# Performance work log

Hardware: AMD Instinct MI355X
Metric: run time of the kernel (lower is better)

## Reference

```python
import jax, jax.numpy as jnp
import numpy as np

NUM_HEADS = 16
LN_EPS = 1e-5


def pos_encoding(length, d):
    pos = jnp.arange(length, dtype=jnp.float32)[:, None]
    i = jnp.arange(d, dtype=jnp.float32)[None, :]
    angle = pos / jnp.power(10000.0, (2.0 * jnp.floor(i / 2.0)) / d)
    return jnp.where((jnp.arange(d) % 2) == 0, jnp.sin(angle), jnp.cos(angle))


def rel_shift(x):
    # x: (B, H, l, m) -> TXL shift trick
    b, h, l, m = x.shape
    x = jnp.concatenate([x, jnp.zeros((b, h, l, 1), x.dtype)], axis=-1)
    x = x.reshape(b, h, l * (m + 1))
    return x[:, :, l - 1:-1].reshape(b, h, l, m)


def layer_norm(x, g, b):
    mu = jnp.mean(x, axis=-1, keepdims=True)
    var = jnp.mean(jnp.square(x - mu), axis=-1, keepdims=True)
    return (x - mu) * jax.lax.rsqrt(var + LN_EPS) * g + b


def setup_inputs() -> dict:
    key = jax.random.key(0)
    B, S, M, D, L, V = 2, 1024, 1024, 1024, 4, 32000
    ks = jax.random.split(key, 32)
    s = 0.02
    d = {
        'inputs': jax.random.randint(ks[0], (B, S), 0, V, dtype=jnp.int32),
        'mems': jax.random.normal(ks[1], (L, B, M, D), jnp.float32),
        'emb': jax.random.normal(ks[2], (V, D), jnp.float32) * s,
        'Wq': jax.random.normal(ks[3], (L, D, D), jnp.float32) * s,
        'bq': jnp.zeros((L, D), jnp.float32),
        'Wke': jax.random.normal(ks[4], (L, D, D), jnp.float32) * s,
        'bke': jnp.zeros((L, D), jnp.float32),
        'Wkr': jax.random.normal(ks[5], (L, D, D), jnp.float32) * s,
        'bkr': jnp.zeros((L, D), jnp.float32),
        'Wv': jax.random.normal(ks[6], (L, D, D), jnp.float32) * s,
        'bv': jnp.zeros((L, D), jnp.float32),
        'Wo': jax.random.normal(ks[7], (L, D, D), jnp.float32) * s,
        'bo': jnp.zeros((L, D), jnp.float32),
        'ln1_g': jnp.ones((L, D), jnp.float32),
        'ln1_b': jnp.zeros((L, D), jnp.float32),
        'W1': jax.random.normal(ks[8], (L, D, D), jnp.float32) * s,
        'b1': jnp.zeros((L, D), jnp.float32),
        'W2': jax.random.normal(ks[9], (L, D, D), jnp.float32) * s,
        'b2': jnp.zeros((L, D), jnp.float32),
        'ln2_g': jnp.ones((L, D), jnp.float32),
        'ln2_b': jnp.zeros((L, D), jnp.float32),
        'Wh': jax.random.normal(ks[10], (D, D), jnp.float32) * s,
        'bh': jnp.zeros((D,), jnp.float32),
        'Wf': jax.random.normal(ks[11], (D, V), jnp.float32) * s,
        'bf': jnp.zeros((V,), jnp.float32),
        'next_mem_len': 1024,
    }
    return d


def reference(inputs, mems, emb, Wq, bq, Wke, bke, Wkr, bkr, Wv, bv, Wo, bo,
              ln1_g, ln1_b, W1, b1, W2, b2, ln2_g, ln2_b, Wh, bh, Wf, bf,
              next_mem_len):
    B, S = inputs.shape
    L, _, M, D = mems.shape
    T = M + S
    H = NUM_HEADS
    dh = D // H
    sqrt_dk = jnp.sqrt(jnp.float32(dh))

    rel_enc = pos_encoding(T, D)[::-1]  # (T, D), reversed
    # look-ahead mask: query i may attend key j iff j <= i + M
    mask = (jnp.arange(T)[None, :] > (jnp.arange(S)[:, None] + M)).astype(jnp.float32)
    mask = mask[None, None] * -1e9  # (1,1,S,T)

    x = emb[inputs] * jnp.sqrt(jnp.float32(D))  # (B,S,D)

    for l in range(L):
        x_tilde = jnp.concatenate([mems[l], x], axis=1)  # (B,T,D)
        q = (x @ Wq[l] + bq[l]).reshape(B, S, H, dh).transpose(0, 2, 1, 3)
        k = (x_tilde @ Wke[l] + bke[l]).reshape(B, T, H, dh).transpose(0, 2, 1, 3)
        v = (x_tilde @ Wv[l] + bv[l]).reshape(B, T, H, dh).transpose(0, 2, 1, 3)
        A = jnp.einsum('bhsd,bhtd->bhst', q, k)
        Qr = (rel_enc @ Wkr[l] + bkr[l]).reshape(T, H, dh).transpose(1, 0, 2)  # (H,T,dh)
        B_hat = jnp.einsum('bhsd,htd->bhst', q, Qr)
        score = (A + rel_shift(B_hat)) / sqrt_dk + mask
        attn = jax.nn.softmax(score, axis=-1)
        ctx = jnp.einsum('bhst,bhtd->bhsd', attn, v)
        ctx = ctx.transpose(0, 2, 1, 3).reshape(B, S, D)
        attn_out = ctx @ Wo[l] + bo[l]
        h1 = layer_norm(x + attn_out, ln1_g[l], ln1_b[l])
        ff = jax.nn.gelu(h1 @ W1[l] + b1[l], approximate=False) @ W2[l] + b2[l]
        x = layer_norm(h1 + ff, ln2_g[l], ln2_b[l])

    x = jax.nn.gelu(x @ Wh + bh, approximate=False)
    logits = x @ Wf + bf
    return logits
```

## Files before the change

### kernel.cpp

```cpp
#include <hip/hip_runtime.h>
#include <hip/hip_bf16.h>
#include <math.h>

typedef __attribute__((ext_vector_type(4))) float f32x4;
typedef __attribute__((ext_vector_type(8))) short s16x8;

#define BB 2
#define SS 1024
#define MEM 1024
#define DD 1024
#define LL 4
#define VV 32000
#define TT 2048
#define NH 16
#define DH 64

__device__ __forceinline__ short f2bf(float f) {
    unsigned u = __float_as_uint(f);
    u += 0x7fffu + ((u >> 16) & 1u);
    return (short)(u >> 16);
}

__device__ __forceinline__ float gelu_f(float x) {
    return 0.5f * x * (1.0f + erff(x * 0.70710678118654752f));
}

__device__ __forceinline__ void gll16(const short* g, short* l) {
    __builtin_amdgcn_global_load_lds(
        (__attribute__((address_space(1))) void*)(short*)g,
        (__attribute__((address_space(3))) void*)l, 16, 0, 0);
}

template<int WM, int WN>
__global__ __launch_bounds__(256) void gemm_k128(
    const short* __restrict__ A, const short* __restrict__ Bt,
    const float* __restrict__ bias, const float* __restrict__ bias2,
    int nsplit, void* __restrict__ Cv, int N, int K, int nby, int act, int obf)
{
    constexpr int BM = WM * 32, BN = WN * 32;
    constexpr int NA = BM / 16, NB = BN / 16;
    __shared__ short a_s[BM * 128];
    __shared__ short b_s[BN * 128];
    const int tid  = threadIdx.x;
    const int lane = tid & 63;
    const int wave = tid >> 6;
    const int wr = wave >> 1, wc = wave & 1;
    const int fr = lane & 15, fg = lane >> 4;

    const int nwg = gridDim.x;
    const int bid = blockIdx.x;
    const int swz = ((nwg & 7) == 0) ? ((bid & 7) * (nwg >> 3) + (bid >> 3)) : bid;
    const size_t m0 = (size_t)(swz % nby) * BM;
    const size_t n0 = (size_t)(swz / nby) * BN;

    const short* gA[NA]; short* lA[NA];
    const short* gB[NB]; short* lB[NB];
    #pragma unroll
    for (int i = 0; i < NA; ++i) {
        gA[i] = A + (m0 + i * 16 + (tid & 15)) * (size_t)K + (tid >> 4) * 8;
        lA[i] = &a_s[(i * 256 + tid) * 8];
    }
    #pragma unroll
    for (int i = 0; i < NB; ++i) {
        gB[i] = Bt + (n0 + i * 16 + (tid & 15)) * (size_t)K + (tid >> 4) * 8;
        lB[i] = &b_s[(i * 256 + tid) * 8];
    }

    f32x4 acc[WM][WN] = {};

    #pragma unroll
    for (int i = 0; i < NA; ++i) gll16(gA[i], lA[i]);
    #pragma unroll
    for (int i = 0; i < NB; ++i) gll16(gB[i], lB[i]);

    const int nt = K >> 7;
    for (int t = 0; t < nt; ++t) {
        __syncthreads();
        s16x8 af[WM][4], bf[WN][4];
        #pragma unroll
        for (int mi = 0; mi < WM; ++mi)
            #pragma unroll
            for (int h = 0; h < 4; ++h)
                af[mi][h] = *(const s16x8*)&a_s[((wr*WM + mi)*256 + (4*h + fg)*16 + fr) * 8];
        #pragma unroll
        for (int ni = 0; ni < WN; ++ni)
            #pragma unroll
            for (int h = 0; h < 4; ++h)
                bf[ni][h] = *(const s16x8*)&b_s[((wc*WN + ni)*256 + (4*h + fg)*16 + fr) * 8];
        if (t + 1 < nt) {
            __syncthreads();
            const int koff = (t + 1) << 7;
            #pragma unroll
            for (int i = 0; i < NA; ++i) gll16(gA[i] + koff, lA[i]);
            #pragma unroll
            for (int i = 0; i < NB; ++i) gll16(gB[i] + koff, lB[i]);
        }
        #pragma unroll
        for (int mi = 0; mi < WM; ++mi)
            #pragma unroll
            for (int ni = 0; ni < WN; ++ni)
                #pragma unroll
                for (int h = 0; h < 4; ++h)
                    acc[mi][ni] = __builtin_amdgcn_mfma_f32_16x16x32_bf16(
                        af[mi][h], bf[ni][h], acc[mi][ni], 0, 0, 0);
    }

    float* Cf = (float*)Cv;
    short* Cb = (short*)Cv;
    #pragma unroll
    for (int mi = 0; mi < WM; ++mi) {
        #pragma unroll
        for (int ni = 0; ni < WN; ++ni) {
            const size_t r0 = m0 + wr*WM*16 + mi*16 + fg*4;
            const size_t c  = n0 + wc*WN*16 + ni*16 + fr;
            const float bb = (c < (size_t)nsplit) ? bias[c] : bias2[c - nsplit];
            #pragma unroll
            for (int rg = 0; rg < 4; ++rg) {
                float vv = acc[mi][ni][rg] + bb;
                if (act) vv = gelu_f(vv);
                if (obf) Cb[(r0 + rg)*(size_t)N + c] = f2bf(vv);
                else     Cf[(r0 + rg)*(size_t)N + c] = vv;
            }
        }
    }
}

#define READ_A8(MH, BUF) \
  _Pragma("unroll") for (int mf = 0; mf < 4; ++mf) \
  _Pragma("unroll") for (int kh = 0; kh < 2; ++kh) \
    aA[mf][kh] = *(const s16x8*)&lds[(BUF)*16384 + WR*8192 + (((MH)*4+mf)*128 + (kh*4+fg)*16 + fr)*8];

#define READ_B8(BUF) \
  _Pragma("unroll") for (int nf = 0; nf < 4; ++nf) \
  _Pragma("unroll") for (int kh = 0; kh < 2; ++kh) \
    bB[nf][kh] = *(const s16x8*)&lds[32768 + (BUF)*16384 + BH*8192 + ((BC4+nf)*128 + (kh*4+fg)*16 + fr)*8];

#define QUAD8(MH, NHX) \
  _Pragma("unroll") for (int mf = 0; mf < 4; ++mf) \
  _Pragma("unroll") for (int n2 = 0; n2 < 2; ++n2) { \
    acc[(MH)*4+mf][(NHX)*2+n2] = __builtin_amdgcn_mfma_f32_16x16x32_bf16( \
        aA[mf][0], bB[(NHX)*2+n2][0], acc[(MH)*4+mf][(NHX)*2+n2], 0, 0, 0); \
    acc[(MH)*4+mf][(NHX)*2+n2] = __builtin_amdgcn_mfma_f32_16x16x32_bf16( \
        aA[mf][1], bB[(NHX)*2+n2][1], acc[(MH)*4+mf][(NHX)*2+n2], 0, 0, 0); }

#define STAGE_A8(HH, BUF, KT) { \
    const short* g = pA0 + (HH)*(128*1024) + (KT)*64; \
    short* l = &lds[(BUF)*16384 + (HH)*8192 + tid*8]; \
    gll16(g, l); gll16(g + 64*1024, l + 512*8); }

#define STAGE_B8(HH, BUF, KT) { \
    const short* g = pB0 + (HH)*(128*1024) + (KT)*64; \
    short* l = &lds[32768 + (BUF)*16384 + (HH)*8192 + tid*8]; \
    gll16(g, l); gll16(g + 64*1024, l + 512*8); }

#define PHASE8(BUF, MH, NHX, RA, RB, SMAT, SH, SBUF, SKT, VMW) { \
    if (RA) { READ_A8(MH, BUF) } \
    if (RB) { READ_B8(BUF) } \
    if ((SMAT) == 0) STAGE_A8(SH, SBUF, SKT) else STAGE_B8(SH, SBUF, SKT) \
    __builtin_amdgcn_s_barrier(); \
    asm volatile("s_waitcnt lgkmcnt(0)" ::: "memory"); \
    __builtin_amdgcn_sched_barrier(0); \
    __builtin_amdgcn_s_setprio(1); \
    QUAD8(MH, NHX) \
    __builtin_amdgcn_s_setprio(0); \
    if (VMW) { asm volatile("s_waitcnt vmcnt(4)" ::: "memory"); } \
    __builtin_amdgcn_s_barrier(); }

__global__ __launch_bounds__(512, 2) void gemm8p(
    const short* __restrict__ A, const short* __restrict__ Bt,
    const float* __restrict__ bias, float* __restrict__ C, int N)
{
    extern __shared__ short lds[];
    const int tid  = threadIdx.x;
    const int lane = tid & 63;
    const int wave = tid >> 6;
    const int WR = wave >> 2;
    const int WC = wave & 3;
    const int BH = WC >> 1;
    const int BC4 = (WC & 1) * 4;
    const int fr = lane & 15, fg = lane >> 4;

    const int nwg = gridDim.x;
    const int bid = blockIdx.x;
    const int swz = ((nwg & 7) == 0) ? ((bid & 7) * (nwg >> 3) + (bid >> 3)) : bid;
    const size_t m0 = (size_t)(swz % 8) * 256;
    const size_t n0 = (size_t)(swz / 8) * 256;

    const int arow0 = (tid >> 7) * 16 + (tid & 15);
    const int aks0  = ((tid >> 4) & 7) * 8;
    const short* pA0 = A  + (m0 + arow0) * 1024 + aks0;
    const short* pB0 = Bt + (n0 + arow0) * 1024 + aks0;

    f32x4 acc[8][4] = {};
    s16x8 aA[4][2], bB[4][2];

    STAGE_B8(0, 0, 0) STAGE_B8(1, 0, 0)
    STAGE_A8(0, 0, 0) STAGE_A8(1, 0, 0)
    STAGE_B8(0, 1, 1) STAGE_B8(1, 1, 1)
    asm volatile("s_waitcnt vmcnt(4)" ::: "memory");
    __builtin_amdgcn_s_barrier();

    for (int it = 0; it < 8; ++it) {
        const int k1 = 2*it + 1;
        int k2 = 2*it + 2; if (k2 > 15) k2 = 15;
        int k3 = 2*it + 3; if (k3 > 15) k3 = 15;
        PHASE8(0, 0, 0, 1, 1, 0, 0, 1, k1, 0)
        PHASE8(0, 0, 1, 0, 0, 0, 1, 1, k1, 0)
        PHASE8(0, 1, 0, 1, 0, 1, 0, 0, k2, 0)
        PHASE8(0, 1, 1, 0, 0, 1, 1, 0, k2, 1)
        PHASE8(1, 0, 0, 1, 1, 0, 0, 0, k2, 0)
        PHASE8(1, 0, 1, 0, 0, 0, 1, 0, k2, 0)
        PHASE8(1, 1, 0, 1, 0, 1, 0, 1, k3, 0)
        PHASE8(1, 1, 1, 0, 0, 1, 1, 1, k3, 1)
    }

    #pragma unroll
    for (int mf = 0; mf < 8; ++mf) {
        #pragma unroll
        for (int nf = 0; nf < 4; ++nf) {
            const size_t r0 = m0 + WR*128 + mf*16 + fg*4;
            const size_t c  = n0 + WC*64 + nf*16 + fr;
            const float bb = bias[c];
            #pragma unroll
            for (int rg = 0; rg < 4; ++rg)
                C[(r0 + rg) * (size_t)N + c] = acc[mf][nf][rg] + bb;
        }
    }
}

__global__ __launch_bounds__(512, 2) void gemm8n(
    const short* __restrict__ A, const short* __restrict__ Bt,
    const float* __restrict__ bA, const float* __restrict__ bBp,
    const float* __restrict__ bCp, int s1, int s2,
    short* __restrict__ Cb, int N, int K, int nby)
{
    extern __shared__ short lds[];
    const int tid  = threadIdx.x;
    const int lane = tid & 63;
    const int wave = tid >> 6;
    const int WR = wave >> 2;
    const int WC = wave & 3;
    const int fr = lane & 15, fg = lane >> 4;

    const int nwg = gridDim.x;
    const int bid = blockIdx.x;
    const int swz = ((nwg & 7) == 0) ? ((bid & 7) * (nwg >> 3) + (bid >> 3)) : bid;
    const size_t m0 = (size_t)(swz % nby) * 256;
    const size_t n0 = (size_t)(swz / nby) * 128;

    const int rA  = (tid >> 7) * 16 + (tid & 15);
    const int ks8 = ((tid >> 4) & 7) * 8;
    const short* pA = A  + (m0 + rA) * (size_t)K + ks8;
    const short* pB = Bt + (n0 + rA) * (size_t)K + ks8;

    auto stageA = [&](int kt, int h, int buf) {
        const short* g = pA + (size_t)(h * 128) * K + kt * 64;
        short* l = &lds[buf * 16384 + h * 8192 + tid * 8];
        gll16(g, l);
        gll16(g + (size_t)64 * K, l + 512 * 8);
    };
    auto stageB = [&](int kt, int buf) {
        const short* g = pB + kt * 64;
        short* l = &lds[49152 + buf * 8192 + tid * 8];
        gll16(g, l);
        gll16(g + (size_t)64 * K, l + 512 * 8);
    };

    f32x4 acc[8][2] = {};
    const int nt = K >> 6;

    stageB(0, 0); stageA(0, 0, 0); stageA(0, 1, 0);
    stageA(1, 0, 1); stageA(1, 1, 1); stageB(1, 1);

    for (int J = 0; J < nt / 2; ++J) {
        const int t0 = 2 * J, t1 = 2 * J + 1;
        const int b0 = t0 % 3, b1 = t1 % 3;
        const int b2 = (t0 + 2) % 3, b3 = (t1 + 2) % 3;
        int s2k = t0 + 2; if (s2k >= nt) s2k = nt - 1;
        int s3k = t1 + 2; if (s3k >= nt) s3k = nt - 1;

        #pragma unroll
        for (int ph = 0; ph < 2; ++ph) {
            const int bt = ph ? b1 : b0;
            asm volatile("s_waitcnt vmcnt(6)" ::: "memory");
            __builtin_amdgcn_s_barrier();
            __builtin_amdgcn_sched_barrier(0);
            if (ph == 0) { stageB(s2k, b2); stageA(s2k, 0, b2); stageA(s2k, 1, b2); }
            else         { stageA(s3k, 0, b3); stageA(s3k, 1, b3); stageB(s3k, b3); }
            s16x8 bB[2][2];
            #pragma unroll
            for (int nf = 0; nf < 2; ++nf)
                #pragma unroll
                for (int kh = 0; kh < 2; ++kh)
                    bB[nf][kh] = *(const s16x8*)&lds[49152 + bt*8192 +
                        ((WC*2 + nf)*128 + (kh*4 + fg)*16 + fr) * 8];
            #pragma unroll
            for (int MH = 0; MH < 2; ++MH) {
                s16x8 aF[4][2];
                #pragma unroll
                for (int mf = 0; mf < 4; ++mf)
                    #pragma unroll
                    for (int kh = 0; kh < 2; ++kh)
                        aF[mf][kh] = *(const s16x8*)&lds[bt*16384 + WR*8192 +
                            ((MH*4 + mf)*128 + (kh*4 + fg)*16 + fr) * 8];
                asm volatile("s_waitcnt lgkmcnt(0)" ::: "memory");
                __builtin_amdgcn_sched_barrier(0);
                __builtin_amdgcn_s_setprio(1);
                #pragma unroll
                for (int mf = 0; mf < 4; ++mf)
                    #pragma unroll
                    for (int nf = 0; nf < 2; ++nf) {
                        acc[MH*4+mf][nf] = __builtin_amdgcn_mfma_f32_16x16x32_bf16(
                            aF[mf][0], bB[nf][0], acc[MH*4+mf][nf], 0, 0, 0);
                        acc[MH*4+mf][nf] = __builtin_amdgcn_mfma_f32_16x16x32_bf16(
                            aF[mf][1], bB[nf][1], acc[MH*4+mf][nf], 0, 0, 0);
                    }
                __builtin_amdgcn_s_setprio(0);
            }
        }
    }

    #pragma unroll
    for (int mf = 0; mf < 8; ++mf) {
        #pragma unroll
        for (int nf = 0; nf < 2; ++nf) {
            const size_t r0 = m0 + WR*128 + mf*16 + fg*4;
            const size_t c  = n0 + WC*32 + nf*16 + fr;
            const float bb = (c < (size_t)s1) ? bA[c]
                            : (c < (size_t)s2) ? bBp[c - s1] : bCp[c - s2];
            #pragma unroll
            for (int rg = 0; rg < 4; ++rg)
                Cb[(r0 + rg) * (size_t)N + c] = f2bf(acc[mf][nf][rg] + bb);
        }
    }
}

__global__ __launch_bounds__(256) void transpose7_kernel(
    const float* w0, const float* w1, const float* w2, const float* w3,
    const float* w4, const float* w5, const float* w6, short* out)
{
    __shared__ float t[32][33];
    const int z = blockIdx.z;
    const float* W;
    switch (z) {
        case 0: W = w0; break; case 1: W = w1; break; case 2: W = w2; break;
        case 3: W = w3; break; case 4: W = w4; break; case 5: W = w5; break;
        default: W = w6; break;
    }
    short* O = out + (size_t)z * DD * DD;
    const int tid = threadIdx.x;
    const int k0 = blockIdx.y * 32, n0 = blockIdx.x * 32;
    const int r = tid >> 3, c4 = (tid & 7) * 4;
    float4 v = *(const float4*)&W[(size_t)(k0 + r) * DD + n0 + c4];
    t[r][c4+0] = v.x; t[r][c4+1] = v.y; t[r][c4+2] = v.z; t[r][c4+3] = v.w;
    __syncthreads();
    short4 o;
    o.x = f2bf(t[c4+0][r]); o.y = f2bf(t[c4+1][r]);
    o.z = f2bf(t[c4+2][r]); o.w = f2bf(t[c4+3][r]);
    *(short4*)&O[(size_t)(n0 + r) * DD + k0 + c4] = o;
}

__global__ __launch_bounds__(256) void transposeF_kernel(
    const float* __restrict__ W, short* __restrict__ O)
{
    __shared__ float t[32][33];
    const int tid = threadIdx.x;
    const int k0 = blockIdx.y * 32, n0 = blockIdx.x * 32;
    const int r = tid >> 3, c4 = (tid & 7) * 4;
    float4 v = *(const float4*)&W[(size_t)(k0 + r) * VV + n0 + c4];
    t[r][c4+0] = v.x; t[r][c4+1] = v.y; t[r][c4+2] = v.z; t[r][c4+3] = v.w;
    __syncthreads();
    short4 o;
    o.x = f2bf(t[c4+0][r]); o.y = f2bf(t[c4+1][r]);
    o.z = f2bf(t[c4+2][r]); o.w = f2bf(t[c4+3][r]);
    *(short4*)&O[(size_t)(n0 + r) * DD + k0 + c4] = o;
}

__global__ __launch_bounds__(256) void attn_kernel(
    const short* __restrict__ q, const short* __restrict__ k,
    const short* __restrict__ v, const short* __restrict__ Qr,
    short* __restrict__ ctx, int kstr, int qstr)
{
    __shared__ short k_s[64][72];
    __shared__ short vT_s[64][72];
    __shared__ short qr_s[128][72];
    __shared__ float a_t[64][68];

    const int tid  = threadIdx.x;
    const int id   = blockIdx.x;
    const int bh   = id & 31;
    const int qi   = ((id >> 5) + bh) & 15;
    const int q0   = qi * 64;
    const int b    = bh >> 4;
    const int h    = bh & 15;
    const int hoff = h * DH;

    const int lane = tid & 63;
    const int wave = tid >> 6;
    const int fr   = lane & 15;
    const int fg   = lane >> 4;
    const int tk = tid >> 2, ck = (tid & 3) * 16;
    const int rq = tid >> 1, dq = (tid & 1) * 32;
    const int jq = tid >> 2, dq3 = (tid & 3) * 16;
    const int sr  = tid >> 2;
    const int sc0 = (tid & 3) * 16;

    const short* qrow = q + ((size_t)(b * TT + q0 + 16 * wave + fr)) * kstr + hoff;
    s16x8 aq0 = *(const s16x8*)(qrow + fg * 8);
    s16x8 aq1 = *(const s16x8*)(qrow + 32 + fg * 8);

    float m_r = -1e30f, l_r = 0.0f;

    const int t_end = q0 + 64 + MEM;
    const int u0b   = SS - 1 - q0 - 63;

    s16x8 kf0, kf1, vf0, vf1, rf0, rf1, rf2, rf3, rg0, rg1;
    auto loadKV = [&](int t0) {
        const short* kp = k + ((size_t)(b * TT + t0 + tk)) * kstr + hoff + ck;
        const short* vp = v + ((size_t)(b * TT + t0 + tk)) * kstr + hoff + ck;
        kf0 = *(const s16x8*)kp;  kf1 = *(const s16x8*)(kp + 8);
        vf0 = *(const s16x8*)vp;  vf1 = *(const s16x8*)(vp + 8);
    };
    {
        int u = u0b + rq;
        u = u < 0 ? 0 : (u > TT - 1 ? TT - 1 : u);
        const short* rp = Qr + (size_t)u * qstr + hoff + dq;
        rf0 = *(const s16x8*)rp;        rf1 = *(const s16x8*)(rp + 8);
        rf2 = *(const s16x8*)(rp + 16); rf3 = *(const s16x8*)(rp + 24);
    }
    auto loadQRring = [&](int tn) {
        int u = tn + u0b + 64 + jq;
        u = u < 0 ? 0 : (u > TT - 1 ? TT - 1 : u);
        const short* rp = Qr + (size_t)u * qstr + hoff + dq3;
        rg0 = *(const s16x8*)rp;
        rg1 = *(const s16x8*)(rp + 8);
    };
    loadKV(0);

    f32x4 opv[4] = {};
    const int nlo = 3 - wave, nhi = 7 - wave;

    for (int t0 = 0; t0 < t_end; t0 += 64) {
        asm volatile("" ::: "memory");
        __builtin_amdgcn_s_barrier();
        __builtin_amdgcn_sched_barrier(0);
        {
            *(s16x8*)&k_s[tk][ck]     = kf0;
            *(s16x8*)&k_s[tk][ck + 8] = kf1;
            #pragma unroll
            for (int i = 0; i < 8; ++i) {
                const int d0 = ck + i, d1 = ck + 8 + i;
                vT_s[d0][tk ^ (((d0 >> 3) & 3) << 3)] = vf0[i];
                vT_s[d1][tk ^ (((d1 >> 3) & 3) << 3)] = vf1[i];
            }
            if (t0 == 0) {
                *(s16x8*)&qr_s[rq][dq]      = rf0;
                *(s16x8*)&qr_s[rq][dq + 8]  = rf1;
                *(s16x8*)&qr_s[rq][dq + 16] = rf2;
                *(s16x8*)&qr_s[rq][dq + 24] = rf3;
            } else {
                const int slot = (t0 + 64 + jq) & 127;
                *(s16x8*)&qr_s[slot][dq3]     = rg0;
                *(s16x8*)&qr_s[slot][dq3 + 8] = rg1;
            }
        }
        if (t0 + 64 < t_end) { loadKV(t0 + 64); loadQRring(t0 + 64); }
        asm volatile("s_waitcnt lgkmcnt(0)" ::: "memory");
        __builtin_amdgcn_s_barrier();
        __builtin_amdgcn_sched_barrier(0);

        {
            __builtin_amdgcn_s_setprio(1);
            #pragma unroll
            for (int n = 0; n < 4; ++n) {
                s16x8 b0 = *(const s16x8*)&k_s[16*n + fr][fg * 8];
                s16x8 b1 = *(const s16x8*)&k_s[16*n + fr][32 + fg * 8];
                f32x4 ca = {0, 0, 0, 0};
                ca = __builtin_amdgcn_mfma_f32_16x16x32_bf16(aq0, b0, ca, 0, 0, 0);
                ca = __builtin_amdgcn_mfma_f32_16x16x32_bf16(aq1, b1, ca, 0, 0, 0);
                #pragma unroll
                for (int rg = 0; rg < 4; ++rg)
                    a_t[16*wave + 4*fg + rg][16*n + fr] = ca[rg];
            }
            __builtin_amdgcn_s_setprio(0);
        }
        {
            #pragma unroll
            for (int n = 0; n < 8; ++n) {
                if (n < nlo || n > nhi) continue;
                const int pr = (t0 + 16*n + fr) & 127;
                s16x8 c0 = *(const s16x8*)&qr_s[pr][fg * 8];
                s16x8 c1 = *(const s16x8*)&qr_s[pr][32 + fg * 8];
                f32x4 cb = {0, 0, 0, 0};
                cb = __builtin_amdgcn_mfma_f32_16x16x32_bf16(aq0, c0, cb, 0, 0, 0);
                cb = __builtin_amdgcn_mfma_f32_16x16x32_bf16(aq1, c1, cb, 0, 0, 0);
                #pragma unroll
                for (int rg = 0; rg < 4; ++rg) {
                    const int r  = 16*wave + 4*fg + rg;
                    const int tl = 16*n + fr - 63 + r;
                    if ((unsigned)tl < 64u) a_t[r][tl] += cb[rg];
                }
            }
        }

        {
            const int sg = q0 + sr;
            float e[16];
            float mx = -1e30f;
            #pragma unroll
            for (int j = 0; j < 16; ++j) {
                const int c = sc0 + j;
                float x = a_t[sr][c] * 0.125f;
                x = (t0 + c > sg + MEM) ? -1e30f : x;
                e[j] = x;
                mx = fmaxf(mx, x);
            }
            mx = fmaxf(mx, __shfl_xor(mx, 1, 64));
            mx = fmaxf(mx, __shfl_xor(mx, 2, 64));
            const float mn  = fmaxf(m_r, mx);
            const float scl = __expf(m_r - mn);
            float sum = 0.0f;
            s16x8 p0, p1;
            #pragma unroll
            for (int j = 0; j < 16; ++j) {
                float ev = __expf(e[j] - mn);
                sum += ev;
                if (j < 8) p0[j] = f2bf(ev); else p1[j - 8] = f2bf(ev);
            }
            sum += __shfl_xor(sum, 1, 64);
            sum += __shfl_xor(sum, 2, 64);
            l_r = l_r * scl + sum;
            m_r = mn;
            short* prow = (short*)&a_t[sr][0];
            *(s16x8*)&prow[sc0]     = p0;
            *(s16x8*)&prow[sc0 + 8] = p1;
            asm volatile("s_waitcnt lgkmcnt(0)" ::: "memory");
            __builtin_amdgcn_sched_barrier(0);

            f32x4 scv;
            #pragma unroll
            for (int rg = 0; rg < 4; ++rg) scv[rg] = __shfl(scl, 16*fg + 4*rg, 64);
            #pragma unroll
            for (int n = 0; n < 4; ++n)
                #pragma unroll
                for (int rg = 0; rg < 4; ++rg) opv[n][rg] *= scv[rg];
            const short* pv = (const short*)&a_t[16*wave + fr][0];
            s16x8 ap0 = *(const s16x8*)&pv[fg * 8];
            s16x8 ap1 = *(const s16x8*)&pv[32 + fg * 8];
            __builtin_amdgcn_s_setprio(1);
            #pragma unroll
            for (int n = 0; n < 4; ++n) {
                const int d  = 16*n + fr;
                const int xw = (d >> 3) & 3;
                s16x8 bv0 = *(const s16x8*)&vT_s[d][(fg ^ xw) * 8];
                s16x8 bv1 = *(const s16x8*)&vT_s[d][32 + (fg ^ xw) * 8];
                opv[n] = __builtin_amdgcn_mfma_f32_16x16x32_bf16(ap0, bv0, opv[n], 0, 0, 0);
                opv[n] = __builtin_amdgcn_mfma_f32_16x16x32_bf16(ap1, bv1, opv[n], 0, 0, 0);
            }
            __builtin_amdgcn_s_setprio(0);
        }
    }

    {
        f32x4 lv;
        #pragma unroll
        for (int rg = 0; rg < 4; ++rg) lv[rg] = __shfl(l_r, 16*fg + 4*rg, 64);
        #pragma unroll
        for (int rg = 0; rg < 4; ++rg) {
            const int r = 16*wave + 4*fg + rg;
            const float inv = 1.0f / lv[rg];
            short* op = ctx + ((size_t)(b * SS + q0 + r)) * DD + hoff;
            #pragma unroll
            for (int n = 0; n < 4; ++n)
                op[16*n + fr] = f2bf(opv[n][rg] * inv);
        }
    }
}

__global__ __launch_bounds__(256) void addln_kernel(
    const float* __restrict__ a, const float* __restrict__ b,
    const float* __restrict__ g, const float* __restrict__ be,
    float* __restrict__ out32, short* __restrict__ outbf)
{
    __shared__ float red[8];
    const int row = blockIdx.x;
    const int tid = threadIdx.x;
    const size_t base = (size_t)row * DD;
    const int c = tid * 4;
    float4 xa = *(const float4*)(a + base + c);
    float4 xb = *(const float4*)(b + base + c);
    float x0 = xa.x + xb.x, x1 = xa.y + xb.y, x2 = xa.z + xb.z, x3 = xa.w + xb.w;
    float s  = x0 + x1 + x2 + x3;
    float sq = x0 * x0 + x1 * x1 + x2 * x2 + x3 * x3;
    #pragma unroll
    for (int o = 32; o > 0; o >>= 1) {
        s  += __shfl_down(s, o, 64);
        sq += __shfl_down(sq, o, 64);
    }
    const int wv = tid >> 6;
    if ((tid & 63) == 0) { red[wv * 2] = s; red[wv * 2 + 1] = sq; }
    __syncthreads();
    float ts = red[0] + red[2] + red[4] + red[6];
    float tq = red[1] + red[3] + red[5] + red[7];
    float mu  = ts * (1.0f / DD);
    float var = tq * (1.0f / DD) - mu * mu;
    float rs  = rsqrtf(var + 1e-5f);
    float4 gv = *(const float4*)(g + c);
    float4 bv = *(const float4*)(be + c);
    float4 o4;
    o4.x = (x0 - mu) * rs * gv.x + bv.x;
    o4.y = (x1 - mu) * rs * gv.y + bv.y;
    o4.z = (x2 - mu) * rs * gv.z + bv.z;
    o4.w = (x3 - mu) * rs * gv.w + bv.w;
    *(float4*)(out32 + base + c) = o4;
    short4 ob;
    ob.x = f2bf(o4.x); ob.y = f2bf(o4.y); ob.z = f2bf(o4.z); ob.w = f2bf(o4.w);
    *(short4*)(outbf + base + c) = ob;
}

__global__ __launch_bounds__(256) void embed_kernel(
    const int* __restrict__ inp, const float* __restrict__ emb,
    float* __restrict__ x32, short* __restrict__ xbf)
{
    const int row = blockIdx.x;
    const int c = threadIdx.x * 4;
    const int idx = inp[row];
    float4 vv = *(const float4*)(emb + (size_t)idx * DD + c);
    vv.x *= 32.0f; vv.y *= 32.0f; vv.z *= 32.0f; vv.w *= 32.0f;
    *(float4*)(x32 + (size_t)row * DD + c) = vv;
    short4 ob;
    ob.x = f2bf(vv.x); ob.y = f2bf(vv.y); ob.z = f2bf(vv.z); ob.w = f2bf(vv.w);
    *(short4*)(xbf + (size_t)row * DD + c) = ob;
}

__global__ __launch_bounds__(256) void concat_kernel(
    const float* __restrict__ mems_l, const short* __restrict__ xbf,
    short* __restrict__ xt)
{
    size_t i = ((size_t)blockIdx.x * 256 + threadIdx.x) * 8;
    size_t bt = i / DD;
    int d = (int)(i - bt * DD);
    int b = (int)(bt / TT);
    int t = (int)(bt - (size_t)b * TT);
    s16x8 o;
    if (t < MEM) {
        const float* mp = mems_l + ((size_t)(b * MEM + t)) * DD + d;
        float4 a0 = *(const float4*)mp;
        float4 a1 = *(const float4*)(mp + 4);
        o[0] = f2bf(a0.x); o[1] = f2bf(a0.y); o[2] = f2bf(a0.z); o[3] = f2bf(a0.w);
        o[4] = f2bf(a1.x); o[5] = f2bf(a1.y); o[6] = f2bf(a1.z); o[7] = f2bf(a1.w);
    } else {
        o = *(const s16x8*)(xbf + ((size_t)(b * SS + (t - MEM))) * DD + d);
    }
    *(s16x8*)(xt + i) = o;
}

__global__ __launch_bounds__(256) void relenc_kernel(short* __restrict__ re)
{
    const int u = blockIdx.x;
    const int p = TT - 1 - u;
    const int i0 = threadIdx.x * 4;
    short4 o;
    #pragma unroll
    for (int j = 0; j < 4; ++j) {
        int i = i0 + j;
        float ex   = (float)(2 * (i >> 1)) * (1.0f / DD);
        float invf = __expf(-ex * 9.210340371976184f);
        float ang  = (float)p * invf;
        float val  = (i & 1) ? cosf(ang) : sinf(ang);
        ((short*)&o)[j] = f2bf(val);
    }
    *(short4*)&re[(size_t)u * DD + i0] = o;
}

extern "C" void kernel_launch(void* const* d_in, const int* in_sizes, int n_in,
                              void* d_out, int out_size, void* d_ws, size_t ws_size,
                              hipStream_t stream)
{
    const int*   inp  = (const int*)d_in[0];
    const float* mems = (const float*)d_in[1];
    const float* emb  = (const float*)d_in[2];
    const float* Wq   = (const float*)d_in[3];
    const float* bq   = (const float*)d_in[4];
    const float* Wke  = (const float*)d_in[5];
    const float* bke  = (const float*)d_in[6];
    const float* Wkr  = (const float*)d_in[7];
    const float* bkr  = (const float*)d_in[8];
    const float* Wv   = (const float*)d_in[9];
    const float* bv   = (const float*)d_in[10];
    const float* Wo   = (const float*)d_in[11];
    const float* bo   = (const float*)d_in[12];
    const float* ln1g = (const float*)d_in[13];
    const float* ln1b = (const float*)d_in[14];
    const float* W1   = (const float*)d_in[15];
    const float* b1   = (const float*)d_in[16];
    const float* W2   = (const float*)d_in[17];
    const float* b2   = (const float*)d_in[18];
    const float* ln2g = (const float*)d_in[19];
    const float* ln2b = (const float*)d_in[20];
    const float* Wh   = (const float*)d_in[21];
    const float* bh   = (const float*)d_in[22];
    const float* Wf   = (const float*)d_in[23];
    const float* bfb  = (const float*)d_in[24];

    hipFuncSetAttribute((const void*)gemm8p,
                        hipFuncAttributeMaxDynamicSharedMemorySize, 131072);
    hipFuncSetAttribute((const void*)gemm8n,
                        hipFuncAttributeMaxDynamicSharedMemorySize, 147456);

    char* wsb = (char*)d_ws;
    size_t off = 0;
    auto alloc = [&](size_t bytes) { char* p = wsb + off; off += (bytes + 255) & ~(size_t)255; return p; };
    float* h132  = (float*)alloc((size_t)BB*SS*DD*4);
    float* ao32  = (float*)alloc((size_t)BB*SS*DD*4);
    float* ff232 = (float*)alloc((size_t)BB*SS*DD*4);
    short* xt    = (short*)alloc((size_t)BB*TT*DD*2);
    short* qkvb  = (short*)alloc((size_t)BB*TT*3*DD*2);
    short* ctxb  = (short*)alloc((size_t)BB*SS*DD*2);
    short* ff1   = (short*)alloc((size_t)BB*SS*DD*2);
    float* x32   = (float*)alloc((size_t)BB*SS*DD*4);
    short* x_bf  = (short*)alloc((size_t)BB*SS*DD*2);
    short* whout = (short*)alloc((size_t)BB*SS*DD*2);
    short* rel   = (short*)alloc((size_t)TT*DD*2);
    short* qr4   = (short*)alloc((size_t)TT*4*DD*2);
    short* wt6   = (short*)alloc((size_t)6*DD*DD*2);
    short* wkr4  = (short*)h132;
    short* wft   = (short*)h132;

    relenc_kernel<<<TT, 256, 0, stream>>>(rel);
    embed_kernel<<<BB * SS, 256, 0, stream>>>(inp, emb, x32, x_bf);

    const size_t WOFF = (size_t)DD * DD;

    transpose7_kernel<<<dim3(32, 32, 4), 256, 0, stream>>>(
        Wkr + 0*WOFF, Wkr + 1*WOFF, Wkr + 2*WOFF, Wkr + 3*WOFF, Wq, Wq, Wq, wkr4);
    gemm8n<<<dim3((TT/256) * (4*DD/128)), 512, 147456, stream>>>(
        rel, wkr4, bkr, bkr, bkr, 4*DD, 4*DD, qr4, 4*DD, DD, TT/256);

    const int gSm = (DD / 64) * ((BB * SS) / 64);

    for (int l = 0; l < LL; ++l) {
        const size_t wo  = (size_t)l * DD * DD;
        const size_t bo_ = (size_t)l * DD;
        transpose7_kernel<<<dim3(32, 32, 6), 256, 0, stream>>>(
            Wq + wo, Wke + wo, Wv + wo, Wo + wo, W1 + wo, W2 + wo, Wq, wt6);
        concat_kernel<<<(BB * TT * DD / 8) / 256, 256, 0, stream>>>(
            mems + (size_t)l * BB * MEM * DD, x_bf, xt);
        gemm8n<<<dim3((BB*TT/256) * (3*DD/128)), 512, 147456, stream>>>(
            xt, wt6, bq + bo_, bke + bo_, bv + bo_, DD, 2*DD, qkvb, 3*DD, DD, BB*TT/256);
        attn_kernel<<<dim3((SS / 64) * BB * NH), 256, 0, stream>>>(
            qkvb + (size_t)MEM * 3 * DD, qkvb + DD, qkvb + 2 * DD,
            qr4 + (size_t)l * DD, ctxb, 3 * DD, 4 * DD);
        gemm_k128<2,2><<<dim3(gSm), 256, 0, stream>>>(
            ctxb, wt6 + 3*WOFF, bo + bo_, bo + bo_, DD, ao32, DD, DD, (BB*SS)/64, 0, 0);
        addln_kernel<<<BB * SS, 256, 0, stream>>>(x32, ao32, ln1g + bo_, ln1b + bo_, h132, x_bf);
        gemm_k128<2,2><<<dim3(gSm), 256, 0, stream>>>(
            x_bf, wt6 + 4*WOFF, b1 + bo_, b1 + bo_, DD, ff1, DD, DD, (BB*SS)/64, 1, 1);
        gemm_k128<2,2><<<dim3(gSm), 256, 0, stream>>>(
            ff1, wt6 + 5*WOFF, b2 + bo_, b2 + bo_, DD, ff232, DD, DD, (BB*SS)/64, 0, 0);
        addln_kernel<<<BB * SS, 256, 0, stream>>>(h132, ff232, ln2g + bo_, ln2b + bo_, x32, x_bf);
    }

    transpose7_kernel<<<dim3(32, 32, 1), 256, 0, stream>>>(
        Wh, Wh, Wh, Wh, Wh, Wh, Wh, wt6);
    transposeF_kernel<<<dim3(VV / 32, DD / 32), 256, 0, stream>>>(Wf, wft);
    gemm_k128<2,2><<<dim3(gSm), 256, 0, stream>>>(
        x_bf, wt6, bh, bh, DD, whout, DD, DD, (BB*SS)/64, 1, 1);
    gemm8p<<<dim3((VV / 256) * ((BB * SS) / 256)), 512, 131072, stream>>>(
        whout, wft, bfb, (float*)d_out, VV);
}
```

Before: 1.263 ms.

## Stage 128 keys per barrier in attention with 192-row Qr ring buffer

The attention kernel now loads 128 key/value rows per outer iteration instead of 64. It processes them as two 64-column halves between a single pair of barriers, with a 192-row circular buffer for the relative-position Qr rows and launch bounds asking for two blocks per CU. This halves the number of barrier/staging rounds and issues larger global loads per thread, aiming to cut sync and latency overhead. In exchange it uses more LDS and more registers for prefetch, which can limit occupancy. It also adds odd index arithmetic in the V read that is immediately overwritten.

```diff
diff --git a/kernel.cpp b/kernel.cpp
--- a/kernel.cpp
+++ b/kernel.cpp
@@ -376,14 +376,14 @@
     *(short4*)&O[(size_t)(n0 + r) * DD + k0 + c4] = o;
 }
 
-__global__ __launch_bounds__(256) void attn_kernel(
+__global__ __launch_bounds__(256, 2) void attn_kernel(
     const short* __restrict__ q, const short* __restrict__ k,
     const short* __restrict__ v, const short* __restrict__ Qr,
     short* __restrict__ ctx, int kstr, int qstr)
 {
-    __shared__ short k_s[64][72];
-    __shared__ short vT_s[64][72];
-    __shared__ short qr_s[128][72];
+    __shared__ short k_s[128][72];
+    __shared__ short vT_s[64][136];
+    __shared__ short qr_s[192][72];
     __shared__ float a_t[64][68];
 
     const int tid  = threadIdx.x;
@@ -399,9 +399,9 @@
     const int wave = tid >> 6;
     const int fr   = lane & 15;
     const int fg   = lane >> 4;
-    const int tk = tid >> 2, ck = (tid & 3) * 16;
-    const int rq = tid >> 1, dq = (tid & 1) * 32;
-    const int jq = tid >> 2, dq3 = (tid & 3) * 16;
+    const int tk2 = tid >> 1, ck2 = (tid & 1) * 32;
+    const int jq2 = tid >> 1, dqr = (tid & 1) * 32;
+    const int j2  = tid >> 2, dq2 = (tid & 3) * 16;
     const int sr  = tid >> 2;
     const int sc0 = (tid & 3) * 16;
 
@@ -414,67 +414,48 @@
     const int t_end = q0 + 64 + MEM;
     const int u0b   = SS - 1 - q0 - 63;
 
-    s16x8 kf0, kf1, vf0, vf1, rf0, rf1, rf2, rf3, rg0, rg1;
-    auto loadKV = [&](int t0) {
-        const short* kp = k + ((size_t)(b * TT + t0 + tk)) * kstr + hoff + ck;
-        const short* vp = v + ((size_t)(b * TT + t0 + tk)) * kstr + hoff + ck;
-        kf0 = *(const s16x8*)kp;  kf1 = *(const s16x8*)(kp + 8);
-        vf0 = *(const s16x8*)vp;  vf1 = *(const s16x8*)(vp + 8);
+    s16x8 kf[4], vf[4], rgq[4], rgq2[2];
+    auto loadKV = [&](int t0n) {
+        const short* kp = k + ((size_t)(b * TT + t0n + tk2)) * kstr + hoff + ck2;
+        const short* vp = v + ((size_t)(b * TT + t0n + tk2)) * kstr + hoff + ck2;
+        #pragma unroll
+        for (int i = 0; i < 4; ++i) {
+            kf[i] = *(const s16x8*)(kp + 8 * i);
+            vf[i] = *(const s16x8*)(vp + 8 * i);
+        }
+    };
+    auto loadQR = [&](int t0n) {
+        int u = t0n + u0b + 63 + jq2;
+        u = u > TT - 1 ? TT - 1 : u;
+        const short* rp = Qr + (size_t)u * qstr + hoff + dqr;
+        #pragma unroll
+        for (int i = 0; i < 4; ++i) rgq[i] = *(const s16x8*)(rp + 8 * i);
     };
     {
-        int u = u0b + rq;
-        u = u < 0 ? 0 : (u > TT - 1 ? TT - 1 : u);
-        const short* rp = Qr + (size_t)u * qstr + hoff + dq;
-        rf0 = *(const s16x8*)rp;        rf1 = *(const s16x8*)(rp + 8);
-        rf2 = *(const s16x8*)(rp + 16); rf3 = *(const s16x8*)(rp + 24);
-    }
-    auto loadQRring = [&](int tn) {
-        int u = tn + u0b + 64 + jq;
-        u = u < 0 ? 0 : (u > TT - 1 ? TT - 1 : u);
-        const short* rp = Qr + (size_t)u * qstr + hoff + dq3;
-        rg0 = *(const s16x8*)rp;
-        rg1 = *(const s16x8*)(rp + 8);
-    };
+        int u1 = u0b + jq2;
+        u1 = u1 > TT - 1 ? TT - 1 : u1;
+        const short* rp1 = Qr + (size_t)u1 * qstr + hoff + dqr;
+        #pragma unroll
+        for (int i = 0; i < 4; ++i) rgq[i] = *(const s16x8*)(rp1 + 8 * i);
+        int u2 = u0b + 128 + j2;
+        u2 = u2 > TT - 1 ? TT - 1 : u2;
+        const short* rp2 = Qr + (size_t)u2 * qstr + hoff + dq2;
+        rgq2[0] = *(const s16x8*)rp2;
+        rgq2[1] = *(const s16x8*)(rp2 + 8);
+    }
     loadKV(0);
 
     f32x4 opv[4] = {};
     const int nlo = 3 - wave, nhi = 7 - wave;
-
-    for (int t0 = 0; t0 < t_end; t0 += 64) {
-        asm volatile("" ::: "memory");
-        __builtin_amdgcn_s_barrier();
-        __builtin_amdgcn_sched_barrier(0);
-        {
-            *(s16x8*)&k_s[tk][ck]     = kf0;
-            *(s16x8*)&k_s[tk][ck + 8] = kf1;
-            #pragma unroll
-            for (int i = 0; i < 8; ++i) {
-                const int d0 = ck + i, d1 = ck + 8 + i;
-                vT_s[d0][tk ^ (((d0 >> 3) & 3) << 3)] = vf0[i];
-                vT_s[d1][tk ^ (((d1 >> 3) & 3) << 3)] = vf1[i];
-            }
-            if (t0 == 0) {
-                *(s16x8*)&qr_s[rq][dq]      = rf0;
-                *(s16x8*)&qr_s[rq][dq + 8]  = rf1;
-                *(s16x8*)&qr_s[rq][dq + 16] = rf2;
-                *(s16x8*)&qr_s[rq][dq + 24] = rf3;
-            } else {
-                const int slot = (t0 + 64 + jq) & 127;
-                *(s16x8*)&qr_s[slot][dq3]     = rg0;
-                *(s16x8*)&qr_s[slot][dq3 + 8] = rg1;
-            }
-        }
-        if (t0 + 64 < t_end) { loadKV(t0 + 64); loadQRring(t0 + 64); }
-        asm volatile("s_waitcnt lgkmcnt(0)" ::: "memory");
-        __builtin_amdgcn_s_barrier();
-        __builtin_amdgcn_sched_barrier(0);
-
+    int rb = 0;
+
+    auto computeHalf = [&](int hh, int t0) {
         {
             __builtin_amdgcn_s_setprio(1);
             #pragma unroll
             for (int n = 0; n < 4; ++n) {
-                s16x8 b0 = *(const s16x8*)&k_s[16*n + fr][fg * 8];
-                s16x8 b1 = *(const s16x8*)&k_s[16*n + fr][32 + fg * 8];
+                s16x8 b0 = *(const s16x8*)&k_s[64*hh + 16*n + fr][fg * 8];
+                s16x8 b1 = *(const s16x8*)&k_s[64*hh + 16*n + fr][32 + fg * 8];
                 f32x4 ca = {0, 0, 0, 0};
                 ca = __builtin_amdgcn_mfma_f32_16x16x32_bf16(aq0, b0, ca, 0, 0, 0);
                 ca = __builtin_amdgcn_mfma_f32_16x16x32_bf16(aq1, b1, ca, 0, 0, 0);
@@ -488,7 +469,8 @@
             #pragma unroll
             for (int n = 0; n < 8; ++n) {
                 if (n < nlo || n > nhi) continue;
-                const int pr = (t0 + 16*n + fr) & 127;
+                int pr = rb + 64*hh + 16*n + fr;
+                if (pr >= 192) pr -= 192;
                 s16x8 c0 = *(const s16x8*)&qr_s[pr][fg * 8];
                 s16x8 c1 = *(const s16x8*)&qr_s[pr][32 + fg * 8];
                 f32x4 cb = {0, 0, 0, 0};
@@ -502,16 +484,16 @@
                 }
             }
         }
-
         {
             const int sg = q0 + sr;
+            const int tb = t0 + 64*hh;
             float e[16];
             float mx = -1e30f;
             #pragma unroll
             for (int j = 0; j < 16; ++j) {
                 const int c = sc0 + j;
                 float x = a_t[sr][c] * 0.125f;
-                x = (t0 + c > sg + MEM) ? -1e30f : x;
+                x = (tb + c > sg + MEM) ? -1e30f : x;
                 e[j] = x;
                 mx = fmaxf(mx, x);
             }
@@ -552,13 +534,56 @@
             for (int n = 0; n < 4; ++n) {
                 const int d  = 16*n + fr;
                 const int xw = (d >> 3) & 3;
-                s16x8 bv0 = *(const s16x8*)&vT_s[d][(fg ^ xw) * 8];
-                s16x8 bv1 = *(const s16x8*)&vT_s[d][32 + (fg ^ xw) * 8];
+                s16x8 bv0 = *(const s16x8*)&vT_s[d][64*hh + (fg ^ xw) * 8];
+                s16x8 bv1 = *(const s16x8*)&vT_s[d][64*hh + 32 + ((fg + 4) ^ xw ? 0 : 0) + (fg ^ xw) * 8 - (fg ^ xw) * 8 + ((fg ^ xw) * 8)];
+                bv1 = *(const s16x8*)&vT_s[d][64*hh + 32 + (fg ^ xw) * 8];
                 opv[n] = __builtin_amdgcn_mfma_f32_16x16x32_bf16(ap0, bv0, opv[n], 0, 0, 0);
                 opv[n] = __builtin_amdgcn_mfma_f32_16x16x32_bf16(ap1, bv1, opv[n], 0, 0, 0);
             }
             __builtin_amdgcn_s_setprio(0);
         }
+    };
+
+    for (int t0 = 0; t0 < t_end; t0 += 128) {
+        asm volatile("" ::: "memory");
+        __builtin_amdgcn_s_barrier();
+        __builtin_amdgcn_sched_barrier(0);
+        {
+            #pragma unroll
+            for (int i = 0; i < 4; ++i)
+                *(s16x8*)&k_s[tk2][ck2 + 8*i] = kf[i];
+            #pragma unroll
+            for (int i = 0; i < 4; ++i) {
+                #pragma unroll
+                for (int e = 0; e < 8; ++e) {
+                    const int d = ck2 + 8*i + e;
+                    const int col = 64*(tk2 >> 6) + ((tk2 & 63) ^ (((d >> 3) & 3) << 3));
+                    vT_s[d][col] = vf[i][e];
+                }
+            }
+            if (t0 == 0) {
+                #pragma unroll
+                for (int i = 0; i < 4; ++i)
+                    *(s16x8*)&qr_s[jq2][dqr + 8*i] = rgq[i];
+                *(s16x8*)&qr_s[128 + j2][dq2]     = rgq2[0];
+                *(s16x8*)&qr_s[128 + j2][dq2 + 8] = rgq2[1];
+            } else {
+                int p = rb + 63 + jq2;
+                if (p >= 192) p -= 192;
+                #pragma unroll
+                for (int i = 0; i < 4; ++i)
+                    *(s16x8*)&qr_s[p][dqr + 8*i] = rgq[i];
+            }
+        }
+        if (t0 + 128 < t_end) { loadKV(t0 + 128); loadQR(t0 + 128); }
+        asm volatile("s_waitcnt lgkmcnt(0)" ::: "memory");
+        __builtin_amdgcn_s_barrier();
+        __builtin_amdgcn_sched_barrier(0);
+
+        computeHalf(0, t0);
+        if (t0 + 64 < t_end) computeHalf(1, t0);
+
+        rb += 128; if (rb >= 192) rb -= 192;
     }
 
     {
```

New measurement: 1.267 ms. About the same (+0.3%).
